# Performance work log

Measured on AMD Instinct MI355X. Metric: run time of the kernel, lower is better.

Reference implementation:

```python
import jax, jax.numpy as jnp
import numpy as np

N = 100000      # nodes
E = 1600000     # edges
F_IN = 64       # num_features
H = 128         # hidden_channels
EPS = 1e-5      # BatchNorm eps


def setup_inputs() -> dict:
    key = jax.random.key(0)
    ks = jax.random.split(key, 24)
    x = jax.random.normal(ks[0], (N, F_IN), dtype=jnp.float32)
    edge_index = jax.random.randint(ks[1], (2, E), 0, N, dtype=jnp.int32)

    def lin(k, fan_in, fan_out):
        return (jax.random.normal(k, (fan_in, fan_out), dtype=jnp.float32)
                * (1.0 / np.sqrt(fan_in)).astype(np.float32))

    def bn(k, c):
        k1, k2, k3, k4 = jax.random.split(k, 4)
        gamma = jax.random.uniform(k1, (c,), minval=0.8, maxval=1.2)
        beta = jax.random.normal(k2, (c,)) * 0.1
        mean = jax.random.normal(k3, (c,)) * 0.1
        var = jax.random.uniform(k4, (c,), minval=0.5, maxval=1.5)
        return gamma, beta, mean, var

    g1, be1, m1, v1 = bn(ks[6], H)
    g2, be2, m2, v2 = bn(ks[7], H)
    return dict(
        x=x, edge_index=edge_index,
        W1=lin(ks[2], F_IN, H), b1=jnp.zeros((H,), jnp.float32),
        g1=g1, be1=be1, m1=m1, v1=v1,
        W2=lin(ks[3], H, H), b2=jnp.zeros((H,), jnp.float32),
        g2=g2, be2=be2, m2=m2, v2=v2,
        W3=lin(ks[4], H, H // 2), b3=jnp.zeros((H // 2,), jnp.float32),
        Wo=lin(ks[5], H // 2, 1), bo=jnp.zeros((1,), jnp.float32),
    )


def _gcn_conv(h_in, W, b, src, dst, dinv):
    # x' = D^{-1/2}(A+I)D^{-1/2} X W + b  (PyG GCNConv with self-loops)
    h = h_in @ W                                   # [N, out]
    norm = (dinv[src] * dinv[dst])[:, None]        # [E, 1]
    msg = h[src] * norm                            # gather: [E, out]
    agg = jax.ops.segment_sum(msg, dst, num_segments=N)  # scatter-add
    return agg + h * (dinv * dinv)[:, None] + b    # self-loop term + bias


def _bn_eval(h, gamma, beta, mean, var):
    return (h - mean) * jax.lax.rsqrt(var + EPS) * gamma + beta


def reference(x, edge_index, W1, b1, g1, be1, m1, v1,
              W2, b2, g2, be2, m2, v2, W3, b3, Wo, bo):
    src, dst = edge_index[0], edge_index[1]
    # degree of A + I (self-loop adds 1)
    deg = jax.ops.segment_sum(jnp.ones((E,), jnp.float32), dst,
                              num_segments=N) + 1.0
    dinv = jax.lax.rsqrt(deg)

    h = _gcn_conv(x, W1, b1, src, dst, dinv)
    h = jax.nn.relu(_bn_eval(h, g1, be1, m1, v1))
    # dropout p=0.5 is identity in eval mode
    h = _gcn_conv(h, W2, b2, src, dst, dinv)
    h = jax.nn.relu(_bn_eval(h, g2, be2, m2, v2))
    h = jax.nn.relu(_gcn_conv(h, W3, b3, src, dst, dinv))
    return h @ Wo + bo  # [N, 1]
```

## Files before the change

kernel.cpp:

```cpp
#include <hip/hip_runtime.h>

#define NN 100000
#define NE 1600000
#define BN_EPS 1e-5f

#define NBUC 196
#define CBLK 391
#define AEPB 4096
#define XS_BLOCKS 782
#define WPREP_BLOCKS 32

typedef _Float16 h2 __attribute__((ext_vector_type(2)));
typedef _Float16 f16x8 __attribute__((ext_vector_type(8)));
typedef float f32x4 __attribute__((ext_vector_type(4)));

static __device__ __forceinline__ unsigned int pack2f(float a, float b) {
    h2 p; p[0] = (_Float16)a; p[1] = (_Float16)b;
    return __builtin_bit_cast(unsigned int, p);
}
static __device__ __forceinline__ float2 unpack2f(unsigned int u) {
    h2 p = __builtin_bit_cast(h2, u);
    return make_float2((float)p[0], (float)p[1]);
}
static __device__ __forceinline__ float unpack1f(unsigned short u) {
    return (float)__builtin_bit_cast(_Float16, u);
}
static __device__ __forceinline__ unsigned short pack1f(float a) {
    return __builtin_bit_cast(unsigned short, (_Float16)a);
}

__global__ __launch_bounds__(1024) void k_hist_cast(
        const int* __restrict__ dst, int* __restrict__ g_hist,
        const float* __restrict__ x, unsigned short* __restrict__ xs,
        const float* __restrict__ W1, const float* __restrict__ W2,
        const float* __restrict__ W3, unsigned short* __restrict__ Wf1,
        unsigned short* __restrict__ Wf2, unsigned short* __restrict__ Wf3) {
    int b = blockIdx.x, t = threadIdx.x;
    if (b < CBLK) {
        __shared__ int h[NBUC];
        if (t < NBUC) h[t] = 0;
        __syncthreads();
        int e0 = b * AEPB;
#pragma unroll
        for (int j = 0; j < 4; ++j) {
            int e = e0 + t + j * 1024;
            if (e < NE) {
                int d = __builtin_nontemporal_load(&dst[e]);
                atomicAdd(&h[d >> 9], 1);
            }
        }
        __syncthreads();
        if (t < NBUC) g_hist[t * CBLK + b] = h[t];
    } else if (b < CBLK + XS_BLOCKS) {
        int i = (b - CBLK) * 1024 + t;
        if (i < NN * 8) {
            int row = i >> 3, c8 = i & 7;
            const float4* xp = (const float4*)(x + (size_t)row * 64 + c8 * 8);
            float4 f0 = xp[0], f1 = xp[1];
            uint4 o;
            o.x = pack2f(f0.x, f0.y); o.y = pack2f(f0.z, f0.w);
            o.z = pack2f(f1.x, f1.y); o.w = pack2f(f1.z, f1.w);
            *(uint4*)(xs + (size_t)row * 64 + c8 * 8) = o;
        }
    } else {
        int i = (b - CBLK - XS_BLOCKS) * 1024 + t;
        if (i < 8192) {
            int j = i & 7, lane = (i >> 3) & 63, ksct = i >> 9;
            int ks = ksct & 1, ct = ksct >> 1;
            int n = ct * 16 + (lane & 15);
            int k = ks * 32 + (lane >> 4) * 8 + j;
            Wf1[i] = pack1f(W1[k * 128 + n]);
        } else if (i < 24576) {
            int q = i - 8192;
            int j = q & 7, lane = (q >> 3) & 63, ksct = q >> 9;
            int ks = ksct & 3, ct = ksct >> 2;
            int n = ct * 16 + (lane & 15);
            int k = ks * 32 + (lane >> 4) * 8 + j;
            Wf2[q] = pack1f(W2[k * 128 + n]);
        } else if (i < 32768) {
            int q = i - 24576;
            int j = q & 7, lane = (q >> 3) & 63, ksct = q >> 9;
            int ks = ksct & 3, ct = ksct >> 2;
            int n = ct * 16 + (lane & 15);
            int k = ks * 32 + (lane >> 4) * 8 + j;
            Wf3[q] = pack1f(W3[k * 64 + n]);
        }
    }
}

__global__ __launch_bounds__(512) void k_scan_cols(int* __restrict__ g_hist,
                                                   int* __restrict__ btot) {
    __shared__ int s[512];
    int k = blockIdx.x, t = threadIdx.x;
    int v = (t < CBLK) ? g_hist[k * CBLK + t] : 0;
    s[t] = v;
    for (int o = 1; o < 512; o <<= 1) {
        __syncthreads();
        int xl = (t >= o) ? s[t - o] : 0;
        __syncthreads();
        s[t] += xl;
    }
    __syncthreads();
    if (t < CBLK) g_hist[k * CBLK + t] = s[t] - v;
    if (t == CBLK - 1) btot[k] = s[t];
}

__global__ __launch_bounds__(256) void k_scan_buckets(const int* __restrict__ btot,
                                                      int* __restrict__ bb,
                                                      int* __restrict__ degoff) {
    __shared__ int s[256];
    int t = threadIdx.x;
    int v = (t < NBUC) ? btot[t] : 0;
    s[t] = v;
    for (int o = 1; o < 256; o <<= 1) {
        __syncthreads();
        int xl = (t >= o) ? s[t - o] : 0;
        __syncthreads();
        s[t] += xl;
    }
    __syncthreads();
    if (t < NBUC) bb[t] = s[t] - v;
    if (t == 0) { bb[NBUC] = NE; degoff[NN] = NE; }
}

__global__ __launch_bounds__(1024) void k_scatter_edges(
        const int* __restrict__ src, const int* __restrict__ dst,
        const int* __restrict__ g_hist, const int* __restrict__ bb,
        int* __restrict__ sdst, int* __restrict__ ssrc) {
    __shared__ int cur[NBUC];
    int b = blockIdx.x, t = threadIdx.x;
    if (t < NBUC) cur[t] = bb[t] + g_hist[t * CBLK + b];
    __syncthreads();
    int e0 = b * AEPB;
#pragma unroll
    for (int j = 0; j < 4; ++j) {
        int e = e0 + t + j * 1024;
        if (e < NE) {
            int d = __builtin_nontemporal_load(&dst[e]);
            int s = __builtin_nontemporal_load(&src[e]);
            int p = atomicAdd(&cur[d >> 9], 1);
            sdst[p] = d;
            ssrc[p] = s;
        }
    }
}

__global__ __launch_bounds__(1024) void k_bucket_csr(
        const int* __restrict__ sdst, const int* __restrict__ ssrc,
        const int* __restrict__ bb, int* __restrict__ csr,
        int* __restrict__ degoff, float* __restrict__ dinv,
        unsigned short* __restrict__ xs) {
    __shared__ int cnt[512], off[512];
    __shared__ float sdv[512];
    int k = blockIdx.x, t = threadIdx.x;
    int n0 = k << 9;
    int ebeg = bb[k], eend = bb[k + 1];
    if (t < 512) cnt[t] = 0;
    __syncthreads();
    for (int e = ebeg + t; e < eend; e += 1024)
        atomicAdd(&cnt[sdst[e] - n0], 1);
    __syncthreads();
    int c = (t < 512) ? cnt[t] : 0;
    if (t < 512) off[t] = c;
    for (int o = 1; o < 512; o <<= 1) {
        __syncthreads();
        int xl = (t < 512 && t >= o) ? off[t - o] : 0;
        __syncthreads();
        if (t < 512) off[t] += xl;
    }
    __syncthreads();
    if (t < 512) {
        int excl = off[t] - c;
        float d = rsqrtf((float)c + 1.0f);
        sdv[t] = d;
        int n = n0 + t;
        if (n < NN) {
            degoff[n] = ebeg + excl;
            dinv[n] = d;
        }
        cnt[t] = excl;
    }
    __syncthreads();
    for (int e = ebeg + t; e < eend; e += 1024) {
        int d = sdst[e];
        int s = ssrc[e];
        int p = atomicAdd(&cnt[d - n0], 1);
        csr[ebeg + p] = s;
    }
    for (int i = t; i < 4096; i += 1024) {
        int r = i >> 3;
        int n = n0 + r;
        if (n >= NN) break;
        float d = sdv[r];
        uint4* p = (uint4*)(xs + (size_t)n * 64) + (i & 7);
        uint4 v = *p;
        float2 q0 = unpack2f(v.x), q1 = unpack2f(v.y);
        float2 q2 = unpack2f(v.z), q3 = unpack2f(v.w);
        v.x = pack2f(q0.x * d, q0.y * d);
        v.y = pack2f(q1.x * d, q1.y * d);
        v.z = pack2f(q2.x * d, q2.y * d);
        v.w = pack2f(q3.x * d, q3.y * d);
        *p = v;
    }
}

__global__ __launch_bounds__(256) void k_gather64_f16(
        const unsigned short* __restrict__ xs, const int* __restrict__ off,
        const int* __restrict__ csr, const float* __restrict__ dinv,
        unsigned short* __restrict__ agg) {
    int n = blockIdx.x * 4 + (threadIdx.x >> 6);
    if (n >= NN) return;
    int lane = threadIdx.x & 63;

    int beg = off[n], end = off[n + 1];
    float a0 = 0.f, a1 = 0.f, a2 = 0.f, a3 = 0.f;
    int e = beg;
    for (; e + 8 <= end; e += 8) {
        int s0 = csr[e],     s1 = csr[e + 1], s2 = csr[e + 2], s3 = csr[e + 3];
        int s4 = csr[e + 4], s5 = csr[e + 5], s6 = csr[e + 6], s7 = csr[e + 7];
        unsigned short u0 = xs[(size_t)s0 * 64 + lane];
        unsigned short u1 = xs[(size_t)s1 * 64 + lane];
        unsigned short u2 = xs[(size_t)s2 * 64 + lane];
        unsigned short u3 = xs[(size_t)s3 * 64 + lane];
        unsigned short u4 = xs[(size_t)s4 * 64 + lane];
        unsigned short u5 = xs[(size_t)s5 * 64 + lane];
        unsigned short u6 = xs[(size_t)s6 * 64 + lane];
        unsigned short u7 = xs[(size_t)s7 * 64 + lane];
        a0 += unpack1f(u0); a1 += unpack1f(u1);
        a2 += unpack1f(u2); a3 += unpack1f(u3);
        a0 += unpack1f(u4); a1 += unpack1f(u5);
        a2 += unpack1f(u6); a3 += unpack1f(u7);
    }
    for (; e + 2 <= end; e += 2) {
        a0 += unpack1f(xs[(size_t)csr[e] * 64 + lane]);
        a1 += unpack1f(xs[(size_t)csr[e + 1] * 64 + lane]);
    }
    if (e < end) a0 += unpack1f(xs[(size_t)csr[e] * 64 + lane]);

    float v = (a0 + a1 + a2 + a3 + unpack1f(xs[(size_t)n * 64 + lane])) * dinv[n];
    agg[(size_t)n * 64 + lane] = pack1f(v);
}

__global__ __launch_bounds__(256) void k_gather128_f16(
        const unsigned short* __restrict__ h1, const int* __restrict__ off,
        const int* __restrict__ csr, const float* __restrict__ dinv,
        unsigned short* __restrict__ agg) {
    int n = blockIdx.x * 4 + (threadIdx.x >> 6);
    if (n >= NN) return;
    int lane = threadIdx.x & 63;
    const unsigned int* h = (const unsigned int*)h1;

    int beg = off[n], end = off[n + 1];
    float ax = 0.f, ay = 0.f, bx = 0.f, by = 0.f;
    float cx = 0.f, cy = 0.f, dx = 0.f, dy = 0.f;
    int e = beg;
    for (; e + 8 <= end; e += 8) {
        int s0 = csr[e],     s1 = csr[e + 1], s2 = csr[e + 2], s3 = csr[e + 3];
        int s4 = csr[e + 4], s5 = csr[e + 5], s6 = csr[e + 6], s7 = csr[e + 7];
        unsigned int u0 = h[(size_t)s0 * 64 + lane];
        unsigned int u1 = h[(size_t)s1 * 64 + lane];
        unsigned int u2 = h[(size_t)s2 * 64 + lane];
        unsigned int u3 = h[(size_t)s3 * 64 + lane];
        unsigned int u4 = h[(size_t)s4 * 64 + lane];
        unsigned int u5 = h[(size_t)s5 * 64 + lane];
        unsigned int u6 = h[(size_t)s6 * 64 + lane];
        unsigned int u7 = h[(size_t)s7 * 64 + lane];
        float2 v0 = unpack2f(u0), v1 = unpack2f(u1), v2 = unpack2f(u2), v3 = unpack2f(u3);
        float2 v4 = unpack2f(u4), v5 = unpack2f(u5), v6 = unpack2f(u6), v7 = unpack2f(u7);
        ax += v0.x; ay += v0.y;  bx += v1.x; by += v1.y;
        cx += v2.x; cy += v2.y;  dx += v3.x; dy += v3.y;
        ax += v4.x; ay += v4.y;  bx += v5.x; by += v5.y;
        cx += v6.x; cy += v6.y;  dx += v7.x; dy += v7.y;
    }
    for (; e + 2 <= end; e += 2) {
        float2 v0 = unpack2f(h[(size_t)csr[e] * 64 + lane]);
        float2 v1 = unpack2f(h[(size_t)csr[e + 1] * 64 + lane]);
        ax += v0.x; ay += v0.y;  bx += v1.x; by += v1.y;
    }
    if (e < end) {
        float2 v0 = unpack2f(h[(size_t)csr[e] * 64 + lane]);
        ax += v0.x; ay += v0.y;
    }
    float2 self = unpack2f(h[(size_t)n * 64 + lane]);
    float dn = dinv[n];
    ((unsigned int*)agg)[(size_t)n * 64 + lane] =
        pack2f((ax + bx + cx + dx + self.x) * dn,
               (ay + by + cy + dy + self.y) * dn);
}

template <int K, int M, int EPI>
__global__ __launch_bounds__(256) void k_gemm_mfma(
        const unsigned short* __restrict__ A, const unsigned short* __restrict__ Wf,
        const float* __restrict__ dinv, const float* __restrict__ bias,
        const float* __restrict__ g, const float* __restrict__ be,
        const float* __restrict__ mn, const float* __restrict__ vr,
        unsigned short* __restrict__ outp) {
    constexpr int KS = K / 32;
    constexpr int CT = M / 16;
    __shared__ __align__(16) unsigned short sWf[CT * KS * 64 * 8];
    __shared__ float sSc[M], sSh[M];

    int tid = threadIdx.x;
    {
        const uint4* s = (const uint4*)Wf;
        uint4* d = (uint4*)sWf;
        constexpr int W4 = CT * KS * 64;
#pragma unroll
        for (int i = tid; i < W4; i += 256) d[i] = s[i];
    }
    if constexpr (EPI == 1 || EPI == 2) {
        for (int c = tid; c < M; c += 256) {
            float s = g[c] * rsqrtf(vr[c] + BN_EPS);
            sSc[c] = s;
            sSh[c] = (bias[c] - mn[c]) * s + be[c];
        }
    }
    __syncthreads();

    int wave = tid >> 6, lane = tid & 63;
    int row0 = blockIdx.x * 64 + wave * 16;
    if (row0 >= NN) return;
    int r  = row0 + (lane & 15);
    int kq = lane >> 4;

    f16x8 bf[KS];
#pragma unroll
    for (int ks = 0; ks < KS; ++ks)
        bf[ks] = *(const f16x8*)(A + (size_t)r * K + ks * 32 + kq * 8);

    float dr = dinv[r];
    const f16x8* wfp = (const f16x8*)sWf;
#pragma unroll
    for (int ct = 0; ct < CT; ++ct) {
        f32x4 acc = {0.f, 0.f, 0.f, 0.f};
#pragma unroll
        for (int ks = 0; ks < KS; ++ks)
            acc = __builtin_amdgcn_mfma_f32_16x16x32_f16(
                wfp[(ct * KS + ks) * 64 + lane], bf[ks], acc, 0, 0, 0);

        int c4 = ct * 16 + kq * 4;
        unsigned short* op = outp + (size_t)r * M + c4;
        if constexpr (EPI == 1 || EPI == 2) {
            float v0 = fmaxf(acc[0] * sSc[c4 + 0] + sSh[c4 + 0], 0.f);
            float v1 = fmaxf(acc[1] * sSc[c4 + 1] + sSh[c4 + 1], 0.f);
            float v2 = fmaxf(acc[2] * sSc[c4 + 2] + sSh[c4 + 2], 0.f);
            float v3 = fmaxf(acc[3] * sSc[c4 + 3] + sSh[c4 + 3], 0.f);
            if constexpr (EPI == 1) { v0 *= dr; v1 *= dr; v2 *= dr; v3 *= dr; }
            uint2 o; o.x = pack2f(v0, v1); o.y = pack2f(v2, v3);
            *(uint2*)op = o;
        } else {
            uint2 o;
            o.x = pack2f(acc[0] * dr, acc[1] * dr);
            o.y = pack2f(acc[2] * dr, acc[3] * dr);
            *(uint2*)op = o;
        }
    }
}

__global__ __launch_bounds__(256) void k_gather_final_f16(
        const unsigned short* __restrict__ hs, const int* __restrict__ off,
        const int* __restrict__ csr, const float* __restrict__ dinv,
        const float* __restrict__ b, const float* __restrict__ Wo,
        const float* __restrict__ bo, float* __restrict__ out) {
    int n = blockIdx.x * 4 + (threadIdx.x >> 6);
    if (n >= NN) return;
    int lane = threadIdx.x & 63;

    int beg = off[n], end = off[n + 1];
    float a0 = 0.f, a1 = 0.f, a2 = 0.f, a3 = 0.f;
    int e = beg;
    for (; e + 8 <= end; e += 8) {
        int s0 = csr[e],     s1 = csr[e + 1], s2 = csr[e + 2], s3 = csr[e + 3];
        int s4 = csr[e + 4], s5 = csr[e + 5], s6 = csr[e + 6], s7 = csr[e + 7];
        a0 += unpack1f(hs[(size_t)s0 * 64 + lane]);
        a1 += unpack1f(hs[(size_t)s1 * 64 + lane]);
        a2 += unpack1f(hs[(size_t)s2 * 64 + lane]);
        a3 += unpack1f(hs[(size_t)s3 * 64 + lane]);
        a0 += unpack1f(hs[(size_t)s4 * 64 + lane]);
        a1 += unpack1f(hs[(size_t)s5 * 64 + lane]);
        a2 += unpack1f(hs[(size_t)s6 * 64 + lane]);
        a3 += unpack1f(hs[(size_t)s7 * 64 + lane]);
    }
    for (; e + 2 <= end; e += 2) {
        a0 += unpack1f(hs[(size_t)csr[e] * 64 + lane]);
        a1 += unpack1f(hs[(size_t)csr[e + 1] * 64 + lane]);
    }
    if (e < end) a0 += unpack1f(hs[(size_t)csr[e] * 64 + lane]);

    float val = (a0 + a1 + a2 + a3 + unpack1f(hs[(size_t)n * 64 + lane])) * dinv[n]
                + b[lane];
    val = fmaxf(val, 0.f) * Wo[lane];
#pragma unroll
    for (int o = 32; o > 0; o >>= 1) val += __shfl_down(val, o, 64);
    if (lane == 0) out[n] = val + bo[0];
}

extern "C" void kernel_launch(void* const* d_in, const int* in_sizes, int n_in,
                              void* d_out, int out_size, void* d_ws, size_t ws_size,
                              hipStream_t stream) {
    const float* x   = (const float*)d_in[0];
    const int*   ei  = (const int*)d_in[1];
    const int*   src = ei;
    const int*   dst = ei + NE;
    const float* W1  = (const float*)d_in[2];
    const float* b1  = (const float*)d_in[3];
    const float* g1  = (const float*)d_in[4];
    const float* be1 = (const float*)d_in[5];
    const float* m1  = (const float*)d_in[6];
    const float* v1  = (const float*)d_in[7];
    const float* W2  = (const float*)d_in[8];
    const float* b2  = (const float*)d_in[9];
    const float* g2  = (const float*)d_in[10];
    const float* be2 = (const float*)d_in[11];
    const float* m2  = (const float*)d_in[12];
    const float* v2  = (const float*)d_in[13];
    const float* W3  = (const float*)d_in[14];
    const float* b3  = (const float*)d_in[15];
    const float* Wo  = (const float*)d_in[16];
    const float* bo  = (const float*)d_in[17];
    float* out = (float*)d_out;

    char* ws = (char*)d_ws;
    float* dinv   = (float*)(ws + 0);
    int*   degoff = (int*)(ws + 400032);
    int*   bb     = (int*)(ws + 800064);
    int*   btot   = (int*)(ws + 801088);
    int*   g_hist = (int*)(ws + 801920);
    unsigned short* Wf1 = (unsigned short*)(ws + 1108480);
    unsigned short* Wf2 = (unsigned short*)(ws + 1124864);
    unsigned short* Wf3 = (unsigned short*)(ws + 1157632);
    int*   csr    = (int*)(ws + 1174016);
    char*  S1     = ws + 7574016;
    char*  S2     = ws + 58774016;

    unsigned short* xs    = (unsigned short*)S1;
    unsigned short* h1ps  = (unsigned short*)S1;
    unsigned short* h2p   = (unsigned short*)S1;
    int*            sdst  = (int*)S2;
    int*            ssrc  = (int*)(S2 + 6400000);
    unsigned short* aggX  = (unsigned short*)S2;
    unsigned short* aggH1 = (unsigned short*)S2;
    unsigned short* hs3   = (unsigned short*)S2;

    int gW = (NN + 3) / 4;
    int gG = (NN + 63) / 64;

    k_hist_cast<<<CBLK + XS_BLOCKS + WPREP_BLOCKS, 1024, 0, stream>>>(
        dst, g_hist, x, xs, W1, W2, W3, Wf1, Wf2, Wf3);
    k_scan_cols<<<NBUC, 512, 0, stream>>>(g_hist, btot);
    k_scan_buckets<<<1, 256, 0, stream>>>(btot, bb, degoff);
    k_scatter_edges<<<CBLK, 1024, 0, stream>>>(src, dst, g_hist, bb, sdst, ssrc);
    k_bucket_csr<<<NBUC, 1024, 0, stream>>>(sdst, ssrc, bb, csr, degoff, dinv, xs);

    k_gather64_f16<<<gW, 256, 0, stream>>>(xs, degoff, csr, dinv, aggX);
    k_gemm_mfma<64, 128, 1><<<gG, 256, 0, stream>>>(
        aggX, Wf1, dinv, b1, g1, be1, m1, v1, h1ps);

    k_gather128_f16<<<gW, 256, 0, stream>>>(h1ps, degoff, csr, dinv, aggH1);
    k_gemm_mfma<128, 128, 2><<<gG, 256, 0, stream>>>(
        aggH1, Wf2, dinv, b2, g2, be2, m2, v2, h2p);

    k_gemm_mfma<128, 64, 3><<<gG, 256, 0, stream>>>(
        h2p, Wf3, dinv, nullptr, nullptr, nullptr, nullptr, nullptr, hs3);
    k_gather_final_f16<<<gW, 256, 0, stream>>>(hs3, degoff, csr, dinv,
                                               b3, Wo, bo, out);
}
```

Baseline: 286.9 us.

## Use finer CSR buckets and pack local dst with src into one word

Destination buckets for the CSR build shrink from 512 to 128 nodes, so there are four times as many buckets. That gives `k_bucket_csr` four times as many blocks, and each block does a shorter in-shared-memory scan over 128 counters. The scatter pass now writes one packed int per edge (7-bit local destination in the high bits, 20-bit source) instead of separate dst and src arrays. This halves the intermediate global writes and reads. In exchange, the per-block histograms and column scans grow, and the single-block bucket scan runs with 1024 threads.

```diff
diff --git a/kernel.cpp b/kernel.cpp
--- a/kernel.cpp
+++ b/kernel.cpp
@@ -4,7 +4,8 @@
 #define NE 1600000
 #define BN_EPS 1e-5f
 
-#define NBUC 196
+#define BSH 7
+#define NBUC 782
 #define CBLK 391
 #define AEPB 4096
 #define XS_BLOCKS 782
@@ -38,7 +39,7 @@
     int b = blockIdx.x, t = threadIdx.x;
     if (b < CBLK) {
         __shared__ int h[NBUC];
-        if (t < NBUC) h[t] = 0;
+        for (int i = t; i < NBUC; i += 1024) h[i] = 0;
         __syncthreads();
         int e0 = b * AEPB;
 #pragma unroll
@@ -46,11 +47,11 @@
             int e = e0 + t + j * 1024;
             if (e < NE) {
                 int d = __builtin_nontemporal_load(&dst[e]);
-                atomicAdd(&h[d >> 9], 1);
+                atomicAdd(&h[d >> BSH], 1);
             }
         }
         __syncthreads();
-        if (t < NBUC) g_hist[t * CBLK + b] = h[t];
+        for (int i = t; i < NBUC; i += 1024) g_hist[i * CBLK + b] = h[i];
     } else if (b < CBLK + XS_BLOCKS) {
         int i = (b - CBLK) * 1024 + t;
         if (i < NN * 8) {
@@ -105,14 +106,14 @@
     if (t == CBLK - 1) btot[k] = s[t];
 }
 
-__global__ __launch_bounds__(256) void k_scan_buckets(const int* __restrict__ btot,
-                                                      int* __restrict__ bb,
-                                                      int* __restrict__ degoff) {
-    __shared__ int s[256];
+__global__ __launch_bounds__(1024) void k_scan_buckets(const int* __restrict__ btot,
+                                                       int* __restrict__ bb,
+                                                       int* __restrict__ degoff) {
+    __shared__ int s[1024];
     int t = threadIdx.x;
     int v = (t < NBUC) ? btot[t] : 0;
     s[t] = v;
-    for (int o = 1; o < 256; o <<= 1) {
+    for (int o = 1; o < 1024; o <<= 1) {
         __syncthreads();
         int xl = (t >= o) ? s[t - o] : 0;
         __syncthreads();
@@ -126,10 +127,10 @@
 __global__ __launch_bounds__(1024) void k_scatter_edges(
         const int* __restrict__ src, const int* __restrict__ dst,
         const int* __restrict__ g_hist, const int* __restrict__ bb,
-        int* __restrict__ sdst, int* __restrict__ ssrc) {
+        int* __restrict__ sed) {
     __shared__ int cur[NBUC];
     int b = blockIdx.x, t = threadIdx.x;
-    if (t < NBUC) cur[t] = bb[t] + g_hist[t * CBLK + b];
+    for (int i = t; i < NBUC; i += 1024) cur[i] = bb[i] + g_hist[i * CBLK + b];
     __syncthreads();
     int e0 = b * AEPB;
 #pragma unroll
@@ -138,38 +139,36 @@
         if (e < NE) {
             int d = __builtin_nontemporal_load(&dst[e]);
             int s = __builtin_nontemporal_load(&src[e]);
-            int p = atomicAdd(&cur[d >> 9], 1);
-            sdst[p] = d;
-            ssrc[p] = s;
+            int p = atomicAdd(&cur[d >> BSH], 1);
+            sed[p] = ((d & 127) << 20) | s;
         }
     }
 }
 
 __global__ __launch_bounds__(1024) void k_bucket_csr(
-        const int* __restrict__ sdst, const int* __restrict__ ssrc,
-        const int* __restrict__ bb, int* __restrict__ csr,
-        int* __restrict__ degoff, float* __restrict__ dinv,
-        unsigned short* __restrict__ xs) {
-    __shared__ int cnt[512], off[512];
-    __shared__ float sdv[512];
+        const int* __restrict__ sed, const int* __restrict__ bb,
+        int* __restrict__ csr, int* __restrict__ degoff,
+        float* __restrict__ dinv, unsigned short* __restrict__ xs) {
+    __shared__ int cnt[128], off[128];
+    __shared__ float sdv[128];
     int k = blockIdx.x, t = threadIdx.x;
-    int n0 = k << 9;
+    int n0 = k << BSH;
     int ebeg = bb[k], eend = bb[k + 1];
-    if (t < 512) cnt[t] = 0;
+    if (t < 128) cnt[t] = 0;
     __syncthreads();
     for (int e = ebeg + t; e < eend; e += 1024)
-        atomicAdd(&cnt[sdst[e] - n0], 1);
-    __syncthreads();
-    int c = (t < 512) ? cnt[t] : 0;
-    if (t < 512) off[t] = c;
-    for (int o = 1; o < 512; o <<= 1) {
-        __syncthreads();
-        int xl = (t < 512 && t >= o) ? off[t - o] : 0;
-        __syncthreads();
-        if (t < 512) off[t] += xl;
-    }
-    __syncthreads();
-    if (t < 512) {
+        atomicAdd(&cnt[((unsigned)sed[e]) >> 20], 1);
+    __syncthreads();
+    int c = (t < 128) ? cnt[t] : 0;
+    if (t < 128) off[t] = c;
+    for (int o = 1; o < 128; o <<= 1) {
+        __syncthreads();
+        int xl = (t < 128 && t >= o) ? off[t - o] : 0;
+        __syncthreads();
+        if (t < 128) off[t] += xl;
+    }
+    __syncthreads();
+    if (t < 128) {
         int excl = off[t] - c;
         float d = rsqrtf((float)c + 1.0f);
         sdv[t] = d;
@@ -182,25 +181,25 @@
     }
     __syncthreads();
     for (int e = ebeg + t; e < eend; e += 1024) {
-        int d = sdst[e];
-        int s = ssrc[e];
-        int p = atomicAdd(&cnt[d - n0], 1);
-        csr[ebeg + p] = s;
-    }
-    for (int i = t; i < 4096; i += 1024) {
-        int r = i >> 3;
+        unsigned v = (unsigned)sed[e];
+        int p = atomicAdd(&cnt[v >> 20], 1);
+        csr[ebeg + p] = v & 0xFFFFF;
+    }
+    {
+        int r = t >> 3;
         int n = n0 + r;
-        if (n >= NN) break;
-        float d = sdv[r];
-        uint4* p = (uint4*)(xs + (size_t)n * 64) + (i & 7);
-        uint4 v = *p;
-        float2 q0 = unpack2f(v.x), q1 = unpack2f(v.y);
-        float2 q2 = unpack2f(v.z), q3 = unpack2f(v.w);
-        v.x = pack2f(q0.x * d, q0.y * d);
-        v.y = pack2f(q1.x * d, q1.y * d);
-        v.z = pack2f(q2.x * d, q2.y * d);
-        v.w = pack2f(q3.x * d, q3.y * d);
-        *p = v;
+        if (n < NN) {
+            float d = sdv[r];
+            uint4* p = (uint4*)(xs + (size_t)n * 64) + (t & 7);
+            uint4 v = *p;
+            float2 q0 = unpack2f(v.x), q1 = unpack2f(v.y);
+            float2 q2 = unpack2f(v.z), q3 = unpack2f(v.w);
+            v.x = pack2f(q0.x * d, q0.y * d);
+            v.y = pack2f(q1.x * d, q1.y * d);
+            v.z = pack2f(q2.x * d, q2.y * d);
+            v.w = pack2f(q3.x * d, q3.y * d);
+            *p = v;
+        }
     }
 }
 
@@ -424,20 +423,19 @@
     float* dinv   = (float*)(ws + 0);
     int*   degoff = (int*)(ws + 400032);
     int*   bb     = (int*)(ws + 800064);
-    int*   btot   = (int*)(ws + 801088);
-    int*   g_hist = (int*)(ws + 801920);
-    unsigned short* Wf1 = (unsigned short*)(ws + 1108480);
-    unsigned short* Wf2 = (unsigned short*)(ws + 1124864);
-    unsigned short* Wf3 = (unsigned short*)(ws + 1157632);
-    int*   csr    = (int*)(ws + 1174016);
-    char*  S1     = ws + 7574016;
-    char*  S2     = ws + 58774016;
+    int*   btot   = (int*)(ws + 803264);
+    int*   g_hist = (int*)(ws + 806400);
+    unsigned short* Wf1 = (unsigned short*)(ws + 2029500 + 4);
+    unsigned short* Wf2 = (unsigned short*)(ws + 2045888);
+    unsigned short* Wf3 = (unsigned short*)(ws + 2078656);
+    int*   csr    = (int*)(ws + 2095040);
+    char*  S1     = ws + 8495040;
+    char*  S2     = ws + 59695040;
 
     unsigned short* xs    = (unsigned short*)S1;
     unsigned short* h1ps  = (unsigned short*)S1;
     unsigned short* h2p   = (unsigned short*)S1;
-    int*            sdst  = (int*)S2;
-    int*            ssrc  = (int*)(S2 + 6400000);
+    int*            sed   = (int*)S2;
     unsigned short* aggX  = (unsigned short*)S2;
     unsigned short* aggH1 = (unsigned short*)S2;
     unsigned short* hs3   = (unsigned short*)S2;
@@ -448,9 +446,9 @@
     k_hist_cast<<<CBLK + XS_BLOCKS + WPREP_BLOCKS, 1024, 0, stream>>>(
         dst, g_hist, x, xs, W1, W2, W3, Wf1, Wf2, Wf3);
     k_scan_cols<<<NBUC, 512, 0, stream>>>(g_hist, btot);
-    k_scan_buckets<<<1, 256, 0, stream>>>(btot, bb, degoff);
-    k_scatter_edges<<<CBLK, 1024, 0, stream>>>(src, dst, g_hist, bb, sdst, ssrc);
-    k_bucket_csr<<<NBUC, 1024, 0, stream>>>(sdst, ssrc, bb, csr, degoff, dinv, xs);
+    k_scan_buckets<<<1, 1024, 0, stream>>>(btot, bb, degoff);
+    k_scatter_edges<<<CBLK, 1024, 0, stream>>>(src, dst, g_hist, bb, sed);
+    k_bucket_csr<<<NBUC, 1024, 0, stream>>>(sed, bb, csr, degoff, dinv, xs);
 
     k_gather64_f16<<<gW, 256, 0, stream>>>(xs, degoff, csr, dinv, aggX);
     k_gemm_mfma<64, 128, 1><<<gG, 256, 0, stream>>>(
```

Result: slower. 309.7 us (+8.0%).
